# Optimization experiments

Hardware: AMD Instinct MI355X
Metric: run time of the kernel (lower is better)

The kernel has to match this reference:

```python
import jax, jax.numpy as jnp
import numpy as np

N, E, F_IN, H, MH, C, G = 100000, 3200000, 128, 32, 64, 10, 64

def _seg_sum(data, ids, num):
    return jax.ops.segment_sum(data, ids, num_segments=num)

def gcn_conv(x, row, col, ew, W, b, n):
    # PyG GCNConv: linear first, then self-loops + symmetric edge-weight norm + scatter-add
    h = x @ W  # [N, H]
    loop = jnp.arange(n)
    r = jnp.concatenate([row, loop])
    c = jnp.concatenate([col, loop])
    w = jnp.concatenate([ew, jnp.ones((n,), dtype=ew.dtype)])
    deg = _seg_sum(w, c, n)
    dinv = jnp.where(deg > 0, jax.lax.rsqrt(deg), 0.0)
    norm = dinv[r] * w * dinv[c]  # [E+N]
    out = _seg_sum(norm[:, None] * h[r], c, n)  # scatter to targets
    return out + b

def setup_inputs():
    key = jax.random.key(0)
    ks = jax.random.split(key, 16)
    inp = {
        "x": jax.random.normal(ks[0], (N, F_IN), dtype=jnp.float32),
        "edge_index": jax.random.randint(ks[1], (2, E), 0, N, dtype=jnp.int64),
        "edge_weight": jax.random.uniform(ks[2], (E,), dtype=jnp.float32),
        "batch": jnp.sort(jax.random.randint(ks[3], (N,), 0, G, dtype=jnp.int64)),
    }
    def lin(k, i, o):
        s = 1.0 / np.sqrt(i)
        k1, k2 = jax.random.split(k)
        return (jax.random.uniform(k1, (i, o), minval=-s, maxval=s, dtype=jnp.float32),
                jax.random.uniform(k2, (o,), minval=-s, maxval=s, dtype=jnp.float32))
    inp["W1"], inp["b1"] = lin(ks[4], F_IN, H)
    inp["W2"], inp["b2"] = lin(ks[5], H, H)
    inp["W3"], inp["b3"] = lin(ks[6], H, H)
    inp["Wm0"], inp["bm0"] = lin(ks[7], H, MH)
    inp["Wm1"], inp["bm1"] = lin(ks[8], MH, MH)
    inp["Wout"], inp["bout"] = lin(ks[9], MH, C)
    return inp

def reference(x, edge_index, edge_weight, batch, W1, b1, W2, b2, W3, b3, Wm0, bm0, Wm1, bm1, Wout, bout):
    row, col = edge_index[0], edge_index[1]
    h = jax.nn.relu(gcn_conv(x, row, col, edge_weight, W1, b1, N))
    h = jax.nn.relu(gcn_conv(h, row, col, edge_weight, W2, b2, N))
    h = gcn_conv(h, row, col, edge_weight, W3, b3, N)
    # global mean pool over graphs
    sums = _seg_sum(h, batch, G)
    counts = _seg_sum(jnp.ones((N,), dtype=h.dtype), batch, G)
    g = sums / jnp.maximum(counts, 1.0)[:, None]
    # dropout p=0.5 is identity at inference (training=False)
    g = jax.nn.relu(g @ Wm0 + bm0)
    g = jax.nn.relu(g @ Wm1 + bm1)
    return g @ Wout + bout
```

## Files before the change

kernel.cpp:

```cpp
#include <hip/hip_runtime.h>

#define NN 100000
#define NE 3200000
#define FIN 128
#define HID 32
#define MH  64
#define NC  10
#define NG  64
#define NBKT 782
#define NBLK 512
#define EPB  (NE / NBLK)
#define SCANL (NBKT * NBLK)
#define SRCMASK 0x1FFFF
#define BCAP 5120

typedef float floatx2 __attribute__((ext_vector_type(2)));

__global__ __launch_bounds__(1024)
void hist_bkt(const int* __restrict__ ei, int* __restrict__ cnt2) {
    __shared__ int h[NBKT];
    int tid = threadIdx.x, blk = blockIdx.x;
    for (int b = tid; b < NBKT; b += 1024) h[b] = 0;
    __syncthreads();
    int base = blk * EPB;
    for (int i = tid; i < EPB; i += 1024)
        atomicAdd(&h[ei[NE + base + i] >> 7], 1);
    __syncthreads();
    for (int b = tid; b < NBKT; b += 1024) cnt2[b * NBLK + blk] = h[b];
}

__global__ void scan_block(const int* __restrict__ in, int* __restrict__ out,
                           int* __restrict__ bsum, int n) {
    __shared__ int lds[256];
    int tid = threadIdx.x;
    int base = blockIdx.x * 1024 + tid * 4;
    int v0 = 0, v1 = 0, v2 = 0, v3 = 0;
    if (base + 0 < n) v0 = in[base + 0];
    if (base + 1 < n) v1 = in[base + 1];
    if (base + 2 < n) v2 = in[base + 2];
    if (base + 3 < n) v3 = in[base + 3];
    int s = v0 + v1 + v2 + v3;
    lds[tid] = s;
    __syncthreads();
    for (int off = 1; off < 256; off <<= 1) {
        int val = (tid >= off) ? lds[tid - off] : 0;
        __syncthreads();
        lds[tid] += val;
        __syncthreads();
    }
    int excl = lds[tid] - s;
    if (tid == 255) bsum[blockIdx.x] = lds[255];
    if (base + 0 < n) out[base + 0] = excl;
    if (base + 1 < n) out[base + 1] = excl + v0;
    if (base + 2 < n) out[base + 2] = excl + v0 + v1;
    if (base + 3 < n) out[base + 3] = excl + v0 + v1 + v2;
}

__global__ void scan_top(int* __restrict__ bsum, int nb, float* __restrict__ sc) {
    int lane = threadIdx.x;
    for (int i = lane; i < NG * HID + NG; i += 64) sc[i] = 0.0f;
    int carry = 0;
    for (int base = 0; base < nb; base += 64) {
        int i = base + lane;
        int orig = (i < nb) ? bsum[i] : 0;
        int v = orig;
#pragma unroll
        for (int off = 1; off < 64; off <<= 1) {
            int t = __shfl_up(v, off, 64);
            if (lane >= off) v += t;
        }
        if (i < nb) bsum[i] = carry + v - orig;
        carry += __shfl(v, 63, 64);
    }
}

__global__ __launch_bounds__(1024)
void scatter_bkt(const int* __restrict__ ei, const float* __restrict__ ew,
                 const int* __restrict__ cnt2, const int* __restrict__ scanned,
                 const int* __restrict__ bsum, int2* __restrict__ tre) {
    __shared__ int2 pay[EPB];
    __shared__ int scur[NBKT];
    __shared__ int hexc[NBKT];
    __shared__ int gbase[NBKT];
    int tid = threadIdx.x, blk = blockIdx.x;
    int myh = 0;
    if (tid < NBKT) {
        int idx = tid * NBLK + blk;
        myh = cnt2[idx];
        gbase[tid] = scanned[idx] + bsum[idx >> 10];
        scur[tid] = myh;
    }
    __syncthreads();
    for (int off = 1; off < NBKT; off <<= 1) {
        int v = (tid < NBKT && tid >= off) ? scur[tid - off] : 0;
        __syncthreads();
        if (tid < NBKT) scur[tid] += v;
        __syncthreads();
    }
    if (tid < NBKT) { int ex = scur[tid] - myh; hexc[tid] = ex; scur[tid] = ex; }
    __syncthreads();
    int base = blk * EPB;
    for (int i = tid; i < EPB; i += 1024) {
        int e = base + i;
        int c = ei[NE + e];
        int r = ei[e];
        unsigned int wb = __float_as_uint(ew[e]);
        int b = c >> 7;
        int j = atomicAdd(&scur[b], 1);
        pay[j] = make_int2(r | ((c & 127) << 17) | ((b & 0xFF) << 24),
                           (int)((wb & ~3u) | ((unsigned)b >> 8)));
    }
    __syncthreads();
    for (int j = tid; j < EPB; j += 1024) {
        int2 q = pay[j];
        int b = (int)((((unsigned)q.y & 3u) << 8) | (((unsigned)q.x >> 24) & 0xFFu));
        int pos = gbase[b] + (j - hexc[b]);
        tre[pos] = make_int2(q.x & 0x00FFFFFF, q.y & ~3);
    }
}

__global__ __launch_bounds__(512)
void sort_k(const int2* __restrict__ tre, const int* __restrict__ scanned,
            const int* __restrict__ bsum, unsigned int* __restrict__ srn4,
            int* __restrict__ rowptr, float* __restrict__ dinv) {
    __shared__ int2 ed[BCAP];
    __shared__ int h[128];
    __shared__ float dw[128];
    __shared__ int cur[128];
    int b = blockIdx.x, tid = threadIdx.x;
    int base = scanned[b * NBLK] + bsum[(b * NBLK) >> 10];
    int end = (b == NBKT - 1)
                  ? NE
                  : scanned[(b + 1) * NBLK] + bsum[((b + 1) * NBLK) >> 10];
    int n = end - base;
    bool staged = (n <= BCAP);
    if (tid < 128) { h[tid] = 0; dw[tid] = 0.f; }
    __syncthreads();
    for (int i = tid; i < n; i += 512) {
        int2 q = tre[base + i];
        if (staged) ed[i] = q;
        int key = (q.x >> 17) & 127;
        atomicAdd(&h[key], 1);
        atomicAdd(&dw[key], __int_as_float(q.y));
    }
    __syncthreads();
    if (tid < 64) {
        int lane = tid;
        int carry = 0;
#pragma unroll
        for (int c = 0; c < 2; ++c) {
            int idx = c * 64 + lane;
            int hv = h[idx];
            int v = hv;
#pragma unroll
            for (int off = 1; off < 64; off <<= 1) {
                int t = __shfl_up(v, off, 64);
                if (lane >= off) v += t;
            }
            cur[idx] = base + carry + v - hv;
            int node = b * 128 + idx;
            if (node < NN) {
                rowptr[node] = base + carry + v;
                dinv[node] = rsqrtf(1.0f + dw[idx]);
            }
            carry += __shfl(v, 63, 64);
        }
    }
    __syncthreads();
    for (int i = tid; i < n; i += 512) {
        int2 q = staged ? ed[i] : tre[base + i];
        int key = (q.x >> 17) & 127;
        int pos = atomicAdd(&cur[key], 1);
        unsigned int wb = (unsigned)q.y;
        wb += 0x7FFFu + ((wb >> 16) & 1u);
        srn4[pos] = (unsigned)(q.x & SRCMASK) | (((wb >> 16) & 0x7FFFu) << 17);
    }
}

template <int IN_DIM, bool RELU_IN>
__global__ __launch_bounds__(256)
void linear_k(const float* __restrict__ in, const float* __restrict__ W,
              const float* __restrict__ dinv, unsigned int* __restrict__ tmp8) {
    constexpr int J4 = IN_DIM / 4;
    constexpr int XSS = J4 + 1;
    __shared__ float4 xs[64 * XSS];
    __shared__ float4 wp[IN_DIM * 8];
    int tid = threadIdx.x;
    for (int idx = tid; idx < IN_DIM * 8; idx += 256) {
        int j = idx >> 3, kg = idx & 7;
        const float* wr = W + j * 32 + kg * 4;
        wp[idx] = make_float4(wr[0], wr[1], wr[2], wr[3]);
    }
    int rbase = blockIdx.x * 64;
    const float4* in4 = (const float4*)in;
    for (int idx = tid; idx < 64 * J4; idx += 256) {
        int row = idx / J4, j4 = idx % J4;
        int grow = rbase + row;
        float4 v = (grow < NN) ? in4[(size_t)grow * J4 + j4]
                               : make_float4(0.f, 0.f, 0.f, 0.f);
        if (RELU_IN) {
            v.x = fmaxf(v.x, 0.f); v.y = fmaxf(v.y, 0.f);
            v.z = fmaxf(v.z, 0.f); v.w = fmaxf(v.w, 0.f);
        }
        xs[row * XSS + j4] = v;
    }
    __syncthreads();
    int kg = tid & 7;
    int rp = tid >> 3;
    int r0 = rbase + 2 * rp;
    if (r0 >= NN) return;
    const float4* x0 = &xs[(2 * rp) * XSS];
    const float4* x1 = &xs[(2 * rp + 1) * XSS];
    float a00 = 0, a01 = 0, a02 = 0, a03 = 0;
    float a10 = 0, a11 = 0, a12 = 0, a13 = 0;
#pragma unroll
    for (int j4 = 0; j4 < J4; ++j4) {
        float4 v0 = x0[j4], v1 = x1[j4];
        const float4* wj = &wp[j4 * 4 * 8 + kg];
        float4 w0 = wj[0], w1 = wj[8], w2 = wj[16], w3 = wj[24];
#define LSTEP(VX0, VX1, W4) \
        a00 = fmaf(VX0, W4.x, a00); a01 = fmaf(VX0, W4.y, a01); \
        a02 = fmaf(VX0, W4.z, a02); a03 = fmaf(VX0, W4.w, a03); \
        a10 = fmaf(VX1, W4.x, a10); a11 = fmaf(VX1, W4.y, a11); \
        a12 = fmaf(VX1, W4.z, a12); a13 = fmaf(VX1, W4.w, a13);
        LSTEP(v0.x, v1.x, w0)
        LSTEP(v0.y, v1.y, w1)
        LSTEP(v0.z, v1.z, w2)
        LSTEP(v0.w, v1.w, w3)
#undef LSTEP
    }
    float d0 = dinv[r0], d1 = dinv[r0 + 1];
    a00 *= d0; a01 *= d0; a02 *= d0; a03 *= d0;
    a10 *= d1; a11 *= d1; a12 *= d1; a13 *= d1;
    int q0 = __builtin_amdgcn_cvt_pk_fp8_f32(a00, a01, 0, false);
    q0 = __builtin_amdgcn_cvt_pk_fp8_f32(a02, a03, q0, true);
    int q1 = __builtin_amdgcn_cvt_pk_fp8_f32(a10, a11, 0, false);
    q1 = __builtin_amdgcn_cvt_pk_fp8_f32(a12, a13, q1, true);
    tmp8[r0 * 8 + kg] = (unsigned int)q0;
    tmp8[(r0 + 1) * 8 + kg] = (unsigned int)q1;
}

struct AccR { floatx2 r0, r1, r2, r3, r4, r5, r6, r7; };

#define ACC8(A0,A1,A2,A3,A4,A5,A6,A7, U, W) { \
    floatx2 lo_, hi_; \
    lo_ = __builtin_amdgcn_cvt_pk_f32_fp8(U.x, false); \
    hi_ = __builtin_amdgcn_cvt_pk_f32_fp8(U.x, true); \
    A0 += lo_ * W; A1 += hi_ * W; \
    lo_ = __builtin_amdgcn_cvt_pk_f32_fp8(U.y, false); \
    hi_ = __builtin_amdgcn_cvt_pk_f32_fp8(U.y, true); \
    A2 += lo_ * W; A3 += hi_ * W; \
    lo_ = __builtin_amdgcn_cvt_pk_f32_fp8(U.z, false); \
    hi_ = __builtin_amdgcn_cvt_pk_f32_fp8(U.z, true); \
    A4 += lo_ * W; A5 += hi_ * W; \
    lo_ = __builtin_amdgcn_cvt_pk_f32_fp8(U.w, false); \
    hi_ = __builtin_amdgcn_cvt_pk_f32_fp8(U.w, true); \
    A6 += lo_ * W; A7 += hi_ * W; }

__device__ __forceinline__ AccR agg_core(const unsigned int* __restrict__ srn4,
                                         const int* __restrict__ rowptr,
                                         const unsigned int* __restrict__ tmp8,
                                         int nid, int s, unsigned int cb) {
    const char* t8 = (const char*)tmp8;
    int end = rowptr[nid];
    int start = (nid == 0) ? 0 : rowptr[nid - 1];
    floatx2 a0 = {0.f,0.f}, a1 = {0.f,0.f}, a2 = {0.f,0.f}, a3 = {0.f,0.f};
    floatx2 a4 = {0.f,0.f}, a5 = {0.f,0.f}, a6 = {0.f,0.f}, a7 = {0.f,0.f};
    floatx2 b0 = {0.f,0.f}, b1 = {0.f,0.f}, b2 = {0.f,0.f}, b3 = {0.f,0.f};
    floatx2 b4 = {0.f,0.f}, b5 = {0.f,0.f}, b6 = {0.f,0.f}, b7 = {0.f,0.f};
    int e = start + s;
    for (; e + 24 < end; e += 32) {
        unsigned int p0 = srn4[e];
        unsigned int p1 = srn4[e + 8];
        unsigned int p2 = srn4[e + 16];
        unsigned int p3 = srn4[e + 24];
        uint4 u0 = *(const uint4*)(t8 + (((p0 & SRCMASK) << 5) | cb));
        uint4 u1 = *(const uint4*)(t8 + (((p1 & SRCMASK) << 5) | cb));
        uint4 u2 = *(const uint4*)(t8 + (((p2 & SRCMASK) << 5) | cb));
        uint4 u3 = *(const uint4*)(t8 + (((p3 & SRCMASK) << 5) | cb));
        float w0 = __uint_as_float((p0 >> 1) & 0x7FFF0000u);
        float w1 = __uint_as_float((p1 >> 1) & 0x7FFF0000u);
        float w2 = __uint_as_float((p2 >> 1) & 0x7FFF0000u);
        float w3 = __uint_as_float((p3 >> 1) & 0x7FFF0000u);
        ACC8(a0,a1,a2,a3,a4,a5,a6,a7, u0, w0)
        ACC8(b0,b1,b2,b3,b4,b5,b6,b7, u1, w1)
        ACC8(a0,a1,a2,a3,a4,a5,a6,a7, u2, w2)
        ACC8(b0,b1,b2,b3,b4,b5,b6,b7, u3, w3)
    }
    for (; e < end; e += 8) {
        unsigned int p = srn4[e];
        uint4 u = *(const uint4*)(t8 + (((p & SRCMASK) << 5) | cb));
        float w = __uint_as_float((p >> 1) & 0x7FFF0000u);
        ACC8(a0,a1,a2,a3,a4,a5,a6,a7, u, w)
    }
    a0 += b0; a1 += b1; a2 += b2; a3 += b3;
    a4 += b4; a5 += b5; a6 += b6; a7 += b7;
#define REDM(M) { \
    a0.x += __shfl_xor(a0.x, M, 64); a0.y += __shfl_xor(a0.y, M, 64); \
    a1.x += __shfl_xor(a1.x, M, 64); a1.y += __shfl_xor(a1.y, M, 64); \
    a2.x += __shfl_xor(a2.x, M, 64); a2.y += __shfl_xor(a2.y, M, 64); \
    a3.x += __shfl_xor(a3.x, M, 64); a3.y += __shfl_xor(a3.y, M, 64); \
    a4.x += __shfl_xor(a4.x, M, 64); a4.y += __shfl_xor(a4.y, M, 64); \
    a5.x += __shfl_xor(a5.x, M, 64); a5.y += __shfl_xor(a5.y, M, 64); \
    a6.x += __shfl_xor(a6.x, M, 64); a6.y += __shfl_xor(a6.y, M, 64); \
    a7.x += __shfl_xor(a7.x, M, 64); a7.y += __shfl_xor(a7.y, M, 64); }
    REDM(2) REDM(4) REDM(8)
#undef REDM
    AccR r;
    r.r0 = a0; r.r1 = a1; r.r2 = a2; r.r3 = a3;
    r.r4 = a4; r.r5 = a5; r.r6 = a6; r.r7 = a7;
    return r;
}

#define EPILOGUE16(O0,O1,O2,O3, NID, CB, D, BIAS, A, RELU) { \
    const char* t8_ = (const char*)tmp8; \
    uint4 sv_ = *(const uint4*)(t8_ + (((unsigned)(NID)) << 5) + (CB)); \
    floatx2 s0_ = __builtin_amdgcn_cvt_pk_f32_fp8(sv_.x, false); \
    floatx2 s1_ = __builtin_amdgcn_cvt_pk_f32_fp8(sv_.x, true); \
    floatx2 s2_ = __builtin_amdgcn_cvt_pk_f32_fp8(sv_.y, false); \
    floatx2 s3_ = __builtin_amdgcn_cvt_pk_f32_fp8(sv_.y, true); \
    floatx2 s4_ = __builtin_amdgcn_cvt_pk_f32_fp8(sv_.z, false); \
    floatx2 s5_ = __builtin_amdgcn_cvt_pk_f32_fp8(sv_.z, true); \
    floatx2 s6_ = __builtin_amdgcn_cvt_pk_f32_fp8(sv_.w, false); \
    floatx2 s7_ = __builtin_amdgcn_cvt_pk_f32_fp8(sv_.w, true); \
    const float4* bp_ = (const float4*)(BIAS) + 4 * c; \
    float4 bq0_ = bp_[0], bq1_ = bp_[1], bq2_ = bp_[2], bq3_ = bp_[3]; \
    O0.x = bq0_.x + (D) * (s0_.x + A.r0.x); \
    O0.y = bq0_.y + (D) * (s0_.y + A.r0.y); \
    O0.z = bq0_.z + (D) * (s1_.x + A.r1.x); \
    O0.w = bq0_.w + (D) * (s1_.y + A.r1.y); \
    O1.x = bq1_.x + (D) * (s2_.x + A.r2.x); \
    O1.y = bq1_.y + (D) * (s2_.y + A.r2.y); \
    O1.z = bq1_.z + (D) * (s3_.x + A.r3.x); \
    O1.w = bq1_.w + (D) * (s3_.y + A.r3.y); \
    O2.x = bq2_.x + (D) * (s4_.x + A.r4.x); \
    O2.y = bq2_.y + (D) * (s4_.y + A.r4.y); \
    O2.z = bq2_.z + (D) * (s5_.x + A.r5.x); \
    O2.w = bq2_.w + (D) * (s5_.y + A.r5.y); \
    O3.x = bq3_.x + (D) * (s6_.x + A.r6.x); \
    O3.y = bq3_.y + (D) * (s6_.y + A.r6.y); \
    O3.z = bq3_.z + (D) * (s7_.x + A.r7.x); \
    O3.w = bq3_.w + (D) * (s7_.y + A.r7.y); \
    if (RELU) { \
        O0.x = fmaxf(O0.x, 0.f); O0.y = fmaxf(O0.y, 0.f); \
        O0.z = fmaxf(O0.z, 0.f); O0.w = fmaxf(O0.w, 0.f); \
        O1.x = fmaxf(O1.x, 0.f); O1.y = fmaxf(O1.y, 0.f); \
        O1.z = fmaxf(O1.z, 0.f); O1.w = fmaxf(O1.w, 0.f); \
        O2.x = fmaxf(O2.x, 0.f); O2.y = fmaxf(O2.y, 0.f); \
        O2.z = fmaxf(O2.z, 0.f); O2.w = fmaxf(O2.w, 0.f); \
        O3.x = fmaxf(O3.x, 0.f); O3.y = fmaxf(O3.y, 0.f); \
        O3.z = fmaxf(O3.z, 0.f); O3.w = fmaxf(O3.w, 0.f); \
    } }

__global__ __launch_bounds__(256)
void aggregate(const unsigned int* __restrict__ srn4,
               const int* __restrict__ rowptr,
               const float* __restrict__ dinv,
               const float* __restrict__ bias,
               const unsigned int* __restrict__ tmp8,
               float* __restrict__ h) {
    int tid = threadIdx.x;
    int nid = (blockIdx.x * 256 + tid) >> 4;
    int lane = tid & 63;
    int c = lane & 1, s = (lane >> 1) & 7;
    unsigned int cb = (unsigned int)c * 16u;
    AccR A = agg_core(srn4, rowptr, tmp8, nid, s, cb);
    if ((lane & 14) == 0) {
        float d = dinv[nid];
        float4 o0, o1, o2, o3;
        EPILOGUE16(o0, o1, o2, o3, nid, cb, d, bias, A, false)
        float4* hp = (float4*)(h + (size_t)nid * HID + 16 * c);
        hp[0] = o0; hp[1] = o1; hp[2] = o2; hp[3] = o3;
    }
}

__global__ __launch_bounds__(256)
void agg_lin(const unsigned int* __restrict__ srn4,
             const int* __restrict__ rowptr,
             const float* __restrict__ dinv,
             const float* __restrict__ bias,
             const float* __restrict__ Wn,
             const unsigned int* __restrict__ tmp8,
             unsigned int* __restrict__ tmp8_out) {
    __shared__ float hrow[4][4][HID];
    __shared__ float Wt[32][36];
    int tid = threadIdx.x;
    for (int idx = tid; idx < 1024; idx += 256)
        Wt[idx & 31][idx >> 5] = Wn[idx];
    int nid = (blockIdx.x * 256 + tid) >> 4;
    int wv = tid >> 6;
    int lane = tid & 63;
    int n = (lane >> 4) & 3;
    int c = lane & 1, s = (lane >> 1) & 7;
    unsigned int cb = (unsigned int)c * 16u;
    __syncthreads();
    AccR A = agg_core(srn4, rowptr, tmp8, nid, s, cb);
    float d = dinv[nid];
    if ((lane & 14) == 0) {
        float4 o0, o1, o2, o3;
        EPILOGUE16(o0, o1, o2, o3, nid, cb, d, bias, A, true)
        float4* hp = (float4*)&hrow[wv][n][16 * c];
        hp[0] = o0; hp[1] = o1; hp[2] = o2; hp[3] = o3;
    }
    int j0 = lane & 15;
    const float4* hb = (const float4*)&hrow[wv][n][0];
    float4 h0 = hb[0], h1 = hb[1], h2 = hb[2], h3 = hb[3];
    float4 h4 = hb[4], h5 = hb[5], h6 = hb[6], h7 = hb[7];
    const float4* w0p = (const float4*)&Wt[j0][0];
    const float4* w1p = (const float4*)&Wt[j0 + 16][0];
    float y0 = 0.f, y1 = 0.f;
#define MVSTEP(K, HV) { float4 wa_ = w0p[K]; float4 wb_ = w1p[K]; \
    y0 = fmaf(HV.x, wa_.x, y0); y0 = fmaf(HV.y, wa_.y, y0); \
    y0 = fmaf(HV.z, wa_.z, y0); y0 = fmaf(HV.w, wa_.w, y0); \
    y1 = fmaf(HV.x, wb_.x, y1); y1 = fmaf(HV.y, wb_.y, y1); \
    y1 = fmaf(HV.z, wb_.z, y1); y1 = fmaf(HV.w, wb_.w, y1); }
    MVSTEP(0, h0) MVSTEP(1, h1) MVSTEP(2, h2) MVSTEP(3, h3)
    MVSTEP(4, h4) MVSTEP(5, h5) MVSTEP(6, h6) MVSTEP(7, h7)
#undef MVSTEP
    y0 *= d; y1 *= d;
    float p1 = __shfl_down(y0, 1, 64);
    float p2 = __shfl_down(y0, 2, 64);
    float p3 = __shfl_down(y0, 3, 64);
    float q1 = __shfl_down(y1, 1, 64);
    float q2 = __shfl_down(y1, 2, 64);
    float q3 = __shfl_down(y1, 3, 64);
    if ((j0 & 3) == 0) {
        int t = j0 >> 2;
        int w0 = __builtin_amdgcn_cvt_pk_fp8_f32(y0, p1, 0, false);
        w0 = __builtin_amdgcn_cvt_pk_fp8_f32(p2, p3, w0, true);
        int w1 = __builtin_amdgcn_cvt_pk_fp8_f32(y1, q1, 0, false);
        w1 = __builtin_amdgcn_cvt_pk_fp8_f32(q2, q3, w1, true);
        tmp8_out[nid * 8 + t] = (unsigned int)w0;
        tmp8_out[nid * 8 + 4 + t] = (unsigned int)w1;
    }
}

__global__ void pool_k(const float* __restrict__ h, const int* __restrict__ batch,
                       float* __restrict__ sums, float* __restrict__ counts) {
    int t = blockIdx.x * 256 + threadIdx.x;
    int chunk = t >> 5, k = t & 31;
    int n0 = chunk * 32;
    if (n0 >= NN) return;
    int n1 = min(n0 + 32, NN);
    int g = batch[n0];
    float acc = 0.f, cacc = 0.f;
    for (int i = n0; i < n1; ++i) {
        int gi = batch[i];
        if (gi != g) {
            atomicAdd(&sums[g * HID + k], acc);
            if (k == 0) atomicAdd(&counts[g], cacc);
            g = gi; acc = 0.f; cacc = 0.f;
        }
        acc += h[(size_t)i * HID + k];
        cacc += 1.f;
    }
    atomicAdd(&sums[g * HID + k], acc);
    if (k == 0) atomicAdd(&counts[g], cacc);
}

__global__ __launch_bounds__(64)
void mlp_k(const float* __restrict__ sums, const float* __restrict__ counts,
           const float* __restrict__ Wm0, const float* __restrict__ bm0,
           const float* __restrict__ Wm1, const float* __restrict__ bm1,
           const float* __restrict__ Wout, const float* __restrict__ bout,
           float* __restrict__ out) {
    __shared__ float g0[HID];
    __shared__ float g1[MH];
    __shared__ float g2[MH];
    int g = blockIdx.x;
    int k = threadIdx.x;
    if (k < HID) g0[k] = sums[g * HID + k] / fmaxf(counts[g], 1.0f);
    __syncthreads();
    float acc = bm0[k];
#pragma unroll
    for (int j = 0; j < HID; ++j) acc = fmaf(g0[j], Wm0[j * MH + k], acc);
    g1[k] = fmaxf(acc, 0.f);
    __syncthreads();
    float acc2 = bm1[k];
#pragma unroll
    for (int j = 0; j < MH; ++j) acc2 = fmaf(g1[j], Wm1[j * MH + k], acc2);
    g2[k] = fmaxf(acc2, 0.f);
    __syncthreads();
    if (k < NC) {
        float acc3 = bout[k];
#pragma unroll
        for (int j = 0; j < MH; ++j) acc3 = fmaf(g2[j], Wout[j * NC + k], acc3);
        out[g * NC + k] = acc3;
    }
}

extern "C" void kernel_launch(void* const* d_in, const int* in_sizes, int n_in,
                              void* d_out, int out_size, void* d_ws, size_t ws_size,
                              hipStream_t stream) {
    const float* x    = (const float*)d_in[0];
    const int*   ei   = (const int*)d_in[1];
    const float* ew   = (const float*)d_in[2];
    const int*   batch= (const int*)d_in[3];
    const float* W1   = (const float*)d_in[4];
    const float* b1   = (const float*)d_in[5];
    const float* W2   = (const float*)d_in[6];
    const float* b2   = (const float*)d_in[7];
    const float* W3   = (const float*)d_in[8];
    const float* b3   = (const float*)d_in[9];
    const float* Wm0  = (const float*)d_in[10];
    const float* bm0  = (const float*)d_in[11];
    const float* Wm1  = (const float*)d_in[12];
    const float* bm1  = (const float*)d_in[13];
    const float* Wout = (const float*)d_in[14];
    const float* bout = (const float*)d_in[15];
    float* out = (float*)d_out;

    char* p = (char*)d_ws;
    unsigned int* srn4 = (unsigned int*)p; p += sizeof(unsigned int) * (size_t)NE;
    char*  S   = p;                      p += 12 * (size_t)NE;
    int2*  tre = (int2*)S;
    int*   cnt2    = (int*)(S + sizeof(int2) * (size_t)NE);
    int*   scanned = cnt2 + SCANL;
    unsigned int* tmp8  = (unsigned int*)S;
    unsigned int* tmp8b = tmp8 + (size_t)NN * 8;
    float* hA  = (float*)(S + 2 * (size_t)NN * HID);
    int*   bsum    = (int*)p;            p += sizeof(int) * 512;
    float* dinv    = (float*)p;          p += sizeof(float) * NN;
    int*   rowptr  = (int*)p;            p += sizeof(int) * NN;
    float* sums    = (float*)p;          p += sizeof(float) * NG * HID;
    float* counts  = (float*)p;

    dim3 blk(256);
    const int NB_SCAN = (SCANL + 1023) / 1024;
    const int NB_LIN = (NN + 63) / 64;
    const int NB_AGG = 6250;

    hist_bkt<<<NBLK, 1024, 0, stream>>>(ei, cnt2);
    scan_block<<<NB_SCAN, blk, 0, stream>>>(cnt2, scanned, bsum, SCANL);
    scan_top<<<1, 64, 0, stream>>>(bsum, NB_SCAN, sums);
    scatter_bkt<<<NBLK, 1024, 0, stream>>>(ei, ew, cnt2, scanned, bsum, tre);
    sort_k<<<NBKT, 512, 0, stream>>>(tre, scanned, bsum, srn4, rowptr, dinv);

    linear_k<FIN, false><<<NB_LIN, blk, 0, stream>>>(x, W1, dinv, tmp8);
    agg_lin<<<NB_AGG, blk, 0, stream>>>(srn4, rowptr, dinv, b1, W2, tmp8, tmp8b);
    agg_lin<<<NB_AGG, blk, 0, stream>>>(srn4, rowptr, dinv, b2, W3, tmp8b, tmp8);
    aggregate<<<NB_AGG, blk, 0, stream>>>(srn4, rowptr, dinv, b3, tmp8, hA);

    pool_k<<<391, blk, 0, stream>>>(hA, batch, sums, counts);
    mlp_k<<<NG, 64, 0, stream>>>(sums, counts, Wm0, bm0, Wm1, bm1, Wout, bout, out);
}
```

Before: 369.1 us.

## Fuse final aggregation with mean-pool and merge edge-loop remainder into clamped main loop

The last GCN aggregation now adds its outputs straight into per-graph sums, using an LDS partial-sum reduction when all 16 nodes of a block share a graph and global atomics otherwise. This removes the hA write and the separate pool kernel. Node counts per graph move to a small cnt_k kernel launched early. The edge loop in agg_core drops its scalar remainder loop and instead clamps indices and zeroes weights, so the tail runs through the unrolled path at the cost of some redundant loads.

```diff
diff --git a/kernel.cpp b/kernel.cpp
--- a/kernel.cpp
+++ b/kernel.cpp
@@ -72,6 +72,21 @@
         if (i < nb) bsum[i] = carry + v - orig;
         carry += __shfl(v, 63, 64);
     }
+}
+
+__global__ void cnt_k(const int* __restrict__ batch, float* __restrict__ counts) {
+    int chunk = blockIdx.x * 256 + threadIdx.x;
+    int n0 = chunk * 32;
+    if (n0 >= NN) return;
+    int n1 = min(n0 + 32, NN);
+    int g = batch[n0];
+    float acc = 0.f;
+    for (int i = n0; i < n1; ++i) {
+        int gi = batch[i];
+        if (gi != g) { atomicAdd(&counts[g], acc); g = gi; acc = 0.f; }
+        acc += 1.f;
+    }
+    atomicAdd(&counts[g], acc);
 }
 
 __global__ __launch_bounds__(1024)
@@ -268,30 +283,27 @@
     floatx2 a4 = {0.f,0.f}, a5 = {0.f,0.f}, a6 = {0.f,0.f}, a7 = {0.f,0.f};
     floatx2 b0 = {0.f,0.f}, b1 = {0.f,0.f}, b2 = {0.f,0.f}, b3 = {0.f,0.f};
     floatx2 b4 = {0.f,0.f}, b5 = {0.f,0.f}, b6 = {0.f,0.f}, b7 = {0.f,0.f};
-    int e = start + s;
-    for (; e + 24 < end; e += 32) {
+    int eM = end - 1;
+    for (int e = start + s; e < end; e += 32) {
+        int i1 = min(e + 8, eM);
+        int i2 = min(e + 16, eM);
+        int i3 = min(e + 24, eM);
         unsigned int p0 = srn4[e];
-        unsigned int p1 = srn4[e + 8];
-        unsigned int p2 = srn4[e + 16];
-        unsigned int p3 = srn4[e + 24];
+        unsigned int p1 = srn4[i1];
+        unsigned int p2 = srn4[i2];
+        unsigned int p3 = srn4[i3];
         uint4 u0 = *(const uint4*)(t8 + (((p0 & SRCMASK) << 5) | cb));
         uint4 u1 = *(const uint4*)(t8 + (((p1 & SRCMASK) << 5) | cb));
         uint4 u2 = *(const uint4*)(t8 + (((p2 & SRCMASK) << 5) | cb));
         uint4 u3 = *(const uint4*)(t8 + (((p3 & SRCMASK) << 5) | cb));
         float w0 = __uint_as_float((p0 >> 1) & 0x7FFF0000u);
-        float w1 = __uint_as_float((p1 >> 1) & 0x7FFF0000u);
-        float w2 = __uint_as_float((p2 >> 1) & 0x7FFF0000u);
-        float w3 = __uint_as_float((p3 >> 1) & 0x7FFF0000u);
+        float w1 = (e + 8  <= eM) ? __uint_as_float((p1 >> 1) & 0x7FFF0000u) : 0.f;
+        float w2 = (e + 16 <= eM) ? __uint_as_float((p2 >> 1) & 0x7FFF0000u) : 0.f;
+        float w3 = (e + 24 <= eM) ? __uint_as_float((p3 >> 1) & 0x7FFF0000u) : 0.f;
         ACC8(a0,a1,a2,a3,a4,a5,a6,a7, u0, w0)
         ACC8(b0,b1,b2,b3,b4,b5,b6,b7, u1, w1)
         ACC8(a0,a1,a2,a3,a4,a5,a6,a7, u2, w2)
         ACC8(b0,b1,b2,b3,b4,b5,b6,b7, u3, w3)
-    }
-    for (; e < end; e += 8) {
-        unsigned int p = srn4[e];
-        uint4 u = *(const uint4*)(t8 + (((p & SRCMASK) << 5) | cb));
-        float w = __uint_as_float((p >> 1) & 0x7FFF0000u);
-        ACC8(a0,a1,a2,a3,a4,a5,a6,a7, u, w)
     }
     a0 += b0; a1 += b1; a2 += b2; a3 += b3;
     a4 += b4; a5 += b5; a6 += b6; a7 += b7;
@@ -353,25 +365,53 @@
     } }
 
 __global__ __launch_bounds__(256)
-void aggregate(const unsigned int* __restrict__ srn4,
-               const int* __restrict__ rowptr,
-               const float* __restrict__ dinv,
-               const float* __restrict__ bias,
-               const unsigned int* __restrict__ tmp8,
-               float* __restrict__ h) {
+void agg_pool(const unsigned int* __restrict__ srn4,
+              const int* __restrict__ rowptr,
+              const float* __restrict__ dinv,
+              const float* __restrict__ bias,
+              const unsigned int* __restrict__ tmp8,
+              const int* __restrict__ batch,
+              float* __restrict__ sums) {
+    __shared__ float psum[HID];
     int tid = threadIdx.x;
     int nid = (blockIdx.x * 256 + tid) >> 4;
     int lane = tid & 63;
     int c = lane & 1, s = (lane >> 1) & 7;
     unsigned int cb = (unsigned int)c * 16u;
+    if (tid < HID) psum[tid] = 0.f;
+    int nb0 = blockIdx.x * 16;
+    int g0 = batch[nb0];
+    bool uni = (g0 == batch[nb0 + 15]);
     AccR A = agg_core(srn4, rowptr, tmp8, nid, s, cb);
+    __syncthreads();
     if ((lane & 14) == 0) {
         float d = dinv[nid];
         float4 o0, o1, o2, o3;
         EPILOGUE16(o0, o1, o2, o3, nid, cb, d, bias, A, false)
-        float4* hp = (float4*)(h + (size_t)nid * HID + 16 * c);
-        hp[0] = o0; hp[1] = o1; hp[2] = o2; hp[3] = o3;
-    }
+        if (uni) {
+            int fb = 16 * c;
+            atomicAdd(&psum[fb + 0],  o0.x); atomicAdd(&psum[fb + 1],  o0.y);
+            atomicAdd(&psum[fb + 2],  o0.z); atomicAdd(&psum[fb + 3],  o0.w);
+            atomicAdd(&psum[fb + 4],  o1.x); atomicAdd(&psum[fb + 5],  o1.y);
+            atomicAdd(&psum[fb + 6],  o1.z); atomicAdd(&psum[fb + 7],  o1.w);
+            atomicAdd(&psum[fb + 8],  o2.x); atomicAdd(&psum[fb + 9],  o2.y);
+            atomicAdd(&psum[fb + 10], o2.z); atomicAdd(&psum[fb + 11], o2.w);
+            atomicAdd(&psum[fb + 12], o3.x); atomicAdd(&psum[fb + 13], o3.y);
+            atomicAdd(&psum[fb + 14], o3.z); atomicAdd(&psum[fb + 15], o3.w);
+        } else {
+            float* sp = sums + (size_t)batch[nid] * HID + 16 * c;
+            atomicAdd(&sp[0],  o0.x); atomicAdd(&sp[1],  o0.y);
+            atomicAdd(&sp[2],  o0.z); atomicAdd(&sp[3],  o0.w);
+            atomicAdd(&sp[4],  o1.x); atomicAdd(&sp[5],  o1.y);
+            atomicAdd(&sp[6],  o1.z); atomicAdd(&sp[7],  o1.w);
+            atomicAdd(&sp[8],  o2.x); atomicAdd(&sp[9],  o2.y);
+            atomicAdd(&sp[10], o2.z); atomicAdd(&sp[11], o2.w);
+            atomicAdd(&sp[12], o3.x); atomicAdd(&sp[13], o3.y);
+            atomicAdd(&sp[14], o3.z); atomicAdd(&sp[15], o3.w);
+        }
+    }
+    __syncthreads();
+    if (uni && tid < HID) atomicAdd(&sums[(size_t)g0 * HID + tid], psum[tid]);
 }
 
 __global__ __launch_bounds__(256)
@@ -435,29 +475,6 @@
     }
 }
 
-__global__ void pool_k(const float* __restrict__ h, const int* __restrict__ batch,
-                       float* __restrict__ sums, float* __restrict__ counts) {
-    int t = blockIdx.x * 256 + threadIdx.x;
-    int chunk = t >> 5, k = t & 31;
-    int n0 = chunk * 32;
-    if (n0 >= NN) return;
-    int n1 = min(n0 + 32, NN);
-    int g = batch[n0];
-    float acc = 0.f, cacc = 0.f;
-    for (int i = n0; i < n1; ++i) {
-        int gi = batch[i];
-        if (gi != g) {
-            atomicAdd(&sums[g * HID + k], acc);
-            if (k == 0) atomicAdd(&counts[g], cacc);
-            g = gi; acc = 0.f; cacc = 0.f;
-        }
-        acc += h[(size_t)i * HID + k];
-        cacc += 1.f;
-    }
-    atomicAdd(&sums[g * HID + k], acc);
-    if (k == 0) atomicAdd(&counts[g], cacc);
-}
-
 __global__ __launch_bounds__(64)
 void mlp_k(const float* __restrict__ sums, const float* __restrict__ counts,
            const float* __restrict__ Wm0, const float* __restrict__ bm0,
@@ -518,7 +535,6 @@
     int*   scanned = cnt2 + SCANL;
     unsigned int* tmp8  = (unsigned int*)S;
     unsigned int* tmp8b = tmp8 + (size_t)NN * 8;
-    float* hA  = (float*)(S + 2 * (size_t)NN * HID);
     int*   bsum    = (int*)p;            p += sizeof(int) * 512;
     float* dinv    = (float*)p;          p += sizeof(float) * NN;
     int*   rowptr  = (int*)p;            p += sizeof(int) * NN;
@@ -533,14 +549,14 @@
     hist_bkt<<<NBLK, 1024, 0, stream>>>(ei, cnt2);
     scan_block<<<NB_SCAN, blk, 0, stream>>>(cnt2, scanned, bsum, SCANL);
     scan_top<<<1, 64, 0, stream>>>(bsum, NB_SCAN, sums);
+    cnt_k<<<13, blk, 0, stream>>>(batch, counts);
     scatter_bkt<<<NBLK, 1024, 0, stream>>>(ei, ew, cnt2, scanned, bsum, tre);
     sort_k<<<NBKT, 512, 0, stream>>>(tre, scanned, bsum, srn4, rowptr, dinv);
 
     linear_k<FIN, false><<<NB_LIN, blk, 0, stream>>>(x, W1, dinv, tmp8);
     agg_lin<<<NB_AGG, blk, 0, stream>>>(srn4, rowptr, dinv, b1, W2, tmp8, tmp8b);
     agg_lin<<<NB_AGG, blk, 0, stream>>>(srn4, rowptr, dinv, b2, W3, tmp8b, tmp8);
-    aggregate<<<NB_AGG, blk, 0, stream>>>(srn4, rowptr, dinv, b3, tmp8, hA);
-
-    pool_k<<<391, blk, 0, stream>>>(hA, batch, sums, counts);
+    agg_pool<<<NB_AGG, blk, 0, stream>>>(srn4, rowptr, dinv, b3, tmp8, batch, sums);
+
     mlp_k<<<NG, 64, 0, stream>>>(sums, counts, Wm0, bm0, Wm1, bm1, Wout, bout, out);
 }
```

Result: slower. 383.4 us (+3.9%).
